# Kernel optimization log

Measured on AMD Instinct MI355X. Metric: run time of the kernel, lower is better.

The kernel has to match this reference:

```python
import jax, jax.numpy as jnp
import numpy as np
import math

IN_SRC, IN_DST, OUT, H = 64, 64, 128, 8
DK = OUT // H


def setup_inputs() -> dict:
    key = jax.random.key(0)
    ks = jax.random.split(key, 24)
    f = lambda k, shp, s=0.05: (jax.random.normal(k, shp, dtype=jnp.float32) * s)
    B, n, m = 16, 256, 128
    inp = {
        'h_dst': jax.random.normal(ks[0], (B, n, IN_DST), dtype=jnp.float32),
        'h_src': jax.random.normal(ks[1], (B, m, IN_SRC), dtype=jnp.float32),
        'h_edge': jax.random.normal(ks[2], (B, n, m), dtype=jnp.float32),
        'ope_ma_adj': jax.random.randint(ks[3], (B, n, m), 0, 2, dtype=jnp.int32),
        'ope_oo_adj': jax.random.randint(ks[4], (B, n, n), 0, 2, dtype=jnp.int32),
        'batch_idxes': jnp.arange(B, dtype=jnp.int64),
        'Wq': f(ks[5], (OUT, IN_DST)), 'bq': f(ks[6], (OUT,)),
        'Wk': f(ks[7], (OUT, IN_SRC)), 'bk': f(ks[8], (OUT,)),
        'Wkd': f(ks[9], (OUT, IN_DST)), 'bkd': f(ks[10], (OUT,)),
        'Wke': f(ks[11], (OUT, 1)), 'bke': f(ks[12], (OUT,)),
        'Wv': f(ks[13], (OUT, IN_SRC)), 'bv': f(ks[14], (OUT,)),
        'Wvd': f(ks[15], (OUT, IN_DST)), 'bvd': f(ks[16], (OUT,)),
        'Wa': f(ks[17], (OUT, OUT)), 'ba': f(ks[18], (OUT,)),
        'rel_pri': jnp.ones((2, H), dtype=jnp.float32),
        'rel_att': f(ks[19], (2, H, DK, DK), 0.2),
        'rel_msg': f(ks[20], (2, H, DK, DK), 0.2),
        'skip': jnp.ones((1,), dtype=jnp.float32),
    }
    return inp


def reference(h_dst, h_src, h_edge, ope_ma_adj, ope_oo_adj, batch_idxes,
              Wq, bq, Wk, bk, Wkd, bkd, Wke, bke, Wv, bv, Wvd, bvd, Wa, ba,
              rel_pri, rel_att, rel_msg, skip):
    B = batch_idxes.shape[0]
    n, m = h_dst.shape[1], h_src.shape[1]
    adj_ma = ope_ma_adj[batch_idxes].astype(jnp.float32)  # [B,n,m]
    adj_oo = ope_oo_adj[batch_idxes].astype(jnp.float32)  # [B,n,n]
    inv_sqrt_dk = 1.0 / math.sqrt(DK)
    # torch einsum 'abcd,abdd->abcd' multiplies by the diagonal of the relation matrix
    dA0 = jnp.diagonal(rel_att[0], axis1=-2, axis2=-1)  # [H,DK]
    dA1 = jnp.diagonal(rel_att[1], axis1=-2, axis2=-1)
    dM0 = jnp.diagonal(rel_msg[0], axis1=-2, axis2=-1)
    dM1 = jnp.diagonal(rel_msg[1], axis1=-2, axis2=-1)

    q = (h_dst @ Wq.T + bq).reshape(B, n, H, DK)           # [B,n,H,DK]
    k = ((h_src @ Wk.T + bk).reshape(B, m, H, DK)) * dA0   # [B,m,H,DK]
    scale0 = rel_pri[0] * inv_sqrt_dk                      # [H]
    m_o_att = jnp.einsum('bnhd,bmhd->bnmh', q, k) * scale0

    # edge projection: Linear(1->OUT) on h_edge[...,None]
    edge = (h_edge[..., None] * Wke[:, 0] + bke).reshape(B, n, m, H, DK) * dA0
    ee = jnp.einsum('bnhd,bnmhd->bnmh', q, edge) * scale0
    m_att = jax.nn.leaky_relu(adj_ma[..., None] * m_o_att + ee, 0.1)

    kd = ((h_dst @ Wkd.T + bkd).reshape(B, n, H, DK)) * dA1
    scale1 = rel_pri[1] * inv_sqrt_dk
    o_att = jax.nn.leaky_relu(adj_oo[..., None] * jnp.einsum('bnhd,bmhd->bnmh', q, kd) * scale1, 0.1)

    att = jnp.concatenate([m_att, o_att], axis=2)          # [B,n,m+n,H]
    mask = jnp.concatenate([adj_ma, adj_oo], axis=2)[..., None] == 1
    att = jax.nn.softmax(jnp.where(mask, att, -1e9), axis=2)
    att_m, att_o = att[:, :, :m], att[:, :, m:]

    v = ((h_src @ Wv.T + bv).reshape(B, m, H, DK)) * dM0   # [B,m,H,DK]
    # m_res_msg = edge + v[:,None]; weighted sum over m (no [B,n,m,H,DK] extra alloc)
    a_m = (jnp.einsum('bnmh,bnmhd->bnhd', att_m, edge)
           + jnp.einsum('bnmh,bmhd->bnhd', att_m, v))
    c = ((h_dst @ Wvd.T + bvd).reshape(B, n, H, DK)) * dM1
    # o_res_msg[b,i,j] = c[b,i] + c[b,j]; weighted sum over j
    a_o = (jnp.einsum('bnjh,bjhd->bnhd', att_o, c)
           + att_o.sum(axis=2)[..., None] * c)

    res = (a_m + a_o).reshape(B, n, OUT)
    trans = jax.nn.gelu(res, approximate=False) @ Wa.T + ba
    alpha = jax.nn.sigmoid(skip[0])
    out = trans * alpha + q.reshape(B, n, OUT) * (1.0 - alpha)
    return out
```

## Files before the change

### kernel.cpp

```cpp
#include <hip/hip_runtime.h>
#include <math.h>

#define H 8
#define DK 16
#define OUTC 128
#define INC 64
#define NB 16
#define NN 256
#define NM 128

typedef float f32x4 __attribute__((ext_vector_type(4)));
typedef short s16x4 __attribute__((ext_vector_type(4)));
typedef short s16x8 __attribute__((ext_vector_type(8)));

#if __has_builtin(__builtin_amdgcn_mfma_f32_16x16x16bf16_1k)
__device__ __forceinline__ f32x4 MFMA16(s16x4 a, s16x4 b, f32x4 c) {
    return __builtin_amdgcn_mfma_f32_16x16x16bf16_1k(a, b, c, 0, 0, 0);
}
#else
__device__ __forceinline__ f32x4 MFMA16(s16x4 a, s16x4 b, f32x4 c) {
    s16x8 a8 = {a[0], a[1], a[2], a[3], 0, 0, 0, 0};
    s16x8 b8 = {b[0], b[1], b[2], b[3], 0, 0, 0, 0};
    return __builtin_amdgcn_mfma_f32_16x16x32_bf16(a8, b8, c, 0, 0, 0);
}
#endif

__device__ __forceinline__ unsigned short f2bf(float x) {
    unsigned int u = __float_as_uint(x);
    return (unsigned short)((u + 0x7fffu + ((u >> 16) & 1u)) >> 16);
}
__device__ __forceinline__ float bf2f(unsigned short s) {
    return __uint_as_float(((unsigned int)s) << 16);
}

struct KArgs {
    const float* h_dst; const float* h_src; const float* h_edge;
    const int* adj_ma; const int* adj_oo;
    const float* Wq; const float* bq; const float* Wk; const float* bk;
    const float* Wkd; const float* bkd; const float* Wke; const float* bke;
    const float* Wv; const float* bv; const float* Wvd; const float* bvd;
    const float* Wa; const float* ba;
    const float* rel_pri; const float* rel_att; const float* rel_msg;
    const float* skip;
    float* qbuf; unsigned short* qpk; unsigned short* kpk; unsigned short* vpk;
    unsigned long long* mk; float* outp;
};

__global__ __launch_bounds__(256) void proj_pack_k(KArgs A)
{
    __shared__ float X_s[64 * 68];
    __shared__ float WT_s[64 * 128];

    int t = threadIdx.x;
    int unit = blockIdx.x;

    if (unit >= 256) {
        int w = ((unit - 256) << 2) + (t >> 6);
        int l = t & 63;
        #pragma unroll
        for (int i = 0; i < 16; ++i) {
            int flat = w * 16 + i;
            int row = flat / 6, g = flat - row * 6;
            int a = (g < 2) ? A.adj_ma[(long)row * NM + (g << 6) + l]
                            : A.adj_oo[(long)row * NN + ((g - 2) << 6) + l];
            unsigned long long m = __ballot(a != 0);
            if (l == 0) A.mk[flat] = m;
        }
        return;
    }

    int type, grow0;
    const float *X, *W, *bias;
    if (unit < 64)        { type = 0; grow0 = unit * 64;        X = A.h_dst; W = A.Wq;  bias = A.bq;  }
    else if (unit < 128)  { type = 2; grow0 = (unit-64) * 64;   X = A.h_dst; W = A.Wkd; bias = A.bkd; }
    else if (unit < 192)  { type = 4; grow0 = (unit-128) * 64;  X = A.h_dst; W = A.Wvd; bias = A.bvd; }
    else if (unit < 224)  { type = 1; grow0 = (unit-192) * 64;  X = A.h_src; W = A.Wk;  bias = A.bk;  }
    else                  { type = 3; grow0 = (unit-224) * 64;  X = A.h_src; W = A.Wv;  bias = A.bv;  }

    #pragma unroll
    for (int p = 0; p < 4; ++p) {
        int idx = t + 256 * p;
        int row = idx >> 4, part = idx & 15;
        float4 v = *(const float4*)(X + (long)(grow0 + row) * INC + part * 4);
        *(float4*)(X_s + row * 68 + part * 4) = v;
    }
    #pragma unroll
    for (int p = 0; p < 8; ++p) {
        int idx = t + 256 * p;
        int o = idx >> 4, part = idx & 15;
        float4 v = *(const float4*)(W + (long)o * INC + part * 4);
        int q0 = o >> 2, ob = o & 3;
        WT_s[(part*4+0)*128 + (((q0 ^ ((part*4+0)&31))<<2) + ob)] = v.x;
        WT_s[(part*4+1)*128 + (((q0 ^ ((part*4+1)&31))<<2) + ob)] = v.y;
        WT_s[(part*4+2)*128 + (((q0 ^ ((part*4+2)&31))<<2) + ob)] = v.z;
        WT_s[(part*4+3)*128 + (((q0 ^ ((part*4+3)&31))<<2) + ob)] = v.w;
    }
    __syncthreads();

    int o4 = t & 31;
    int rq = t >> 5;
    float4 acc[8];
    #pragma unroll
    for (int rr = 0; rr < 8; ++rr) acc[rr] = make_float4(0.f, 0.f, 0.f, 0.f);

    #pragma unroll 4
    for (int i4 = 0; i4 < 16; ++i4) {
        float4 w0 = *(const float4*)(WT_s + (i4*4+0)*128 + ((o4 ^ ((i4*4+0)&31))<<2));
        float4 w1 = *(const float4*)(WT_s + (i4*4+1)*128 + ((o4 ^ ((i4*4+1)&31))<<2));
        float4 w2 = *(const float4*)(WT_s + (i4*4+2)*128 + ((o4 ^ ((i4*4+2)&31))<<2));
        float4 w3 = *(const float4*)(WT_s + (i4*4+3)*128 + ((o4 ^ ((i4*4+3)&31))<<2));
        #pragma unroll
        for (int rr = 0; rr < 8; ++rr) {
            float4 x = *(const float4*)(X_s + (rq + 8*rr) * 68 + i4*4);
            acc[rr].x += x.x*w0.x + x.y*w1.x + x.z*w2.x + x.w*w3.x;
            acc[rr].y += x.x*w0.y + x.y*w1.y + x.z*w2.y + x.w*w3.y;
            acc[rr].z += x.x*w0.z + x.y*w1.z + x.z*w2.z + x.w*w3.z;
            acc[rr].w += x.x*w0.w + x.y*w1.w + x.z*w2.w + x.w*w3.w;
        }
    }

    int obase = o4 * 4;
    int head = o4 >> 2;
    float4 bs = *(const float4*)(bias + obase);
    float scl[4];
    #pragma unroll
    for (int c = 0; c < 4; ++c) {
        int o = obase + c;
        int hh = o >> 4, d = o & 15;
        float v = 1.f;
        if (type == 1)      v = A.rel_pri[hh]     * 0.25f * A.rel_att[(hh*DK + d)*DK + d];
        else if (type == 2) v = A.rel_pri[H + hh] * 0.25f * A.rel_att[((H + hh)*DK + d)*DK + d];
        else if (type == 3) v = A.rel_msg[(hh*DK + d)*DK + d];
        else if (type == 4) v = A.rel_msg[((H + hh)*DK + d)*DK + d];
        scl[c] = v;
    }
    #pragma unroll
    for (int rr = 0; rr < 8; ++rr) {
        int grow = grow0 + rq + 8*rr;
        float4 r4;
        r4.x = (acc[rr].x + bs.x) * scl[0];
        r4.y = (acc[rr].y + bs.y) * scl[1];
        r4.z = (acc[rr].z + bs.z) * scl[2];
        r4.w = (acc[rr].w + bs.w) * scl[3];
        if (type == 0) {
            *(float4*)(A.qbuf + (long)grow * OUTC + obase) = r4;
            unsigned int lo = (unsigned int)f2bf(r4.x) | ((unsigned int)f2bf(r4.y) << 16);
            unsigned int hi = (unsigned int)f2bf(r4.z) | ((unsigned int)f2bf(r4.w) << 16);
            int b = grow >> 8, row = grow & 255;
            int lane = ((o4 & 3) << 4) + (row & 15);
            ((uint2*)A.qpk)[(long)((b*H + head)*16 + (row >> 4)) * 64 + lane] = make_uint2(lo, hi);
        } else if (type == 1 || type == 2) {
            unsigned int lo = (unsigned int)f2bf(r4.x) | ((unsigned int)f2bf(r4.y) << 16);
            unsigned int hi = (unsigned int)f2bf(r4.z) | ((unsigned int)f2bf(r4.w) << 16);
            int b, key;
            if (type == 1) { b = grow >> 7; key = grow & 127; }
            else           { b = grow >> 8; key = 128 + (grow & 255); }
            int lane = (key & 15) + ((o4 & 3) << 4);
            ((uint2*)A.kpk)[(long)((b*H + head)*24 + (key >> 4)) * 64 + lane] = make_uint2(lo, hi);
        } else {
            int b, key;
            if (type == 3) { b = grow >> 7; key = grow & 127; }
            else           { b = grow >> 8; key = 128 + (grow & 255); }
            int tt = key >> 4, lg = (key >> 2) & 3, slot = key & 3;
            int dbase = (o4 & 3) * 4;
            unsigned short* vp = A.vpk + ((long)((b*H + head)*24 + tt) * 64) * 4;
            vp[(lg*16 + dbase+0)*4 + slot] = f2bf(r4.x);
            vp[(lg*16 + dbase+1)*4 + slot] = f2bf(r4.y);
            vp[(lg*16 + dbase+2)*4 + slot] = f2bf(r4.z);
            vp[(lg*16 + dbase+3)*4 + slot] = f2bf(r4.w);
        }
    }
}

__global__ __launch_bounds__(512) void attn_out_k(KArgs A)
{
    __shared__ __align__(16) unsigned char smem[73984];
    float* gel_s = (float*)smem;
    float* WaT   = (float*)(smem + 8448);
    float* he_s  = (float*)(smem + 8448);
    unsigned long long* mk_s = (unsigned long long*)(smem + 17152);
    float* s1s2_s = (float*)(smem + 17920);
    float* stats_s = (float*)(smem + 18944);

    int t = threadIdx.x;
    int bid = blockIdx.x;
    int b = bid >> 4;
    int chunk = bid & 15;
    int row0 = b * NN + chunk * 16;

    {
        int q = t >> 5, jc = (t & 31) << 2;
        float4 v = *(const float4*)(A.h_edge + (long)(row0 + q) * NM + jc);
        he_s[(jc+0)*17 + q] = v.x;
        he_s[(jc+1)*17 + q] = v.y;
        he_s[(jc+2)*17 + q] = v.z;
        he_s[(jc+3)*17 + q] = v.w;
    }
    if (t < 96) mk_s[t] = A.mk[(long)row0 * 6 + t];
    if (t < 128) {
        int row = t & 15, hh = t >> 4;
        const float* qr = A.qbuf + (long)(row0 + row) * OUTC + hh * DK;
        float s1 = 0.f, s2 = 0.f;
        #pragma unroll
        for (int d = 0; d < DK; ++d) {
            int o = hh * DK + d;
            float qq = qr[d] * A.rel_att[o * DK + d];
            s1 += qq * A.Wke[o];
            s2 += qq * A.bke[o];
        }
        float sc = A.rel_pri[hh] * 0.25f;
        s1s2_s[(hh*16 + row)*2]     = s1 * sc;
        s1s2_s[(hh*16 + row)*2 + 1] = s2 * sc;
    }
    __syncthreads();

    int w = t >> 6, l = t & 63;
    int qi = l & 15;
    int grpb = (l >> 4) << 2;
    int bh = b * H + w;

    union { uint2 u; s16x4 s; } qf;
    qf.u = ((const uint2*)A.qpk)[(long)(bh * 16 + chunk) * 64 + l];

    float S1q = s1s2_s[(w*16 + qi)*2], S2q = s1s2_s[(w*16 + qi)*2 + 1];
    unsigned int mdw[12];
    #pragma unroll
    for (int i = 0; i < 12; ++i) mdw[i] = ((const unsigned int*)(mk_s + qi * 6))[i];

    const uint2* kbase = (const uint2*)A.kpk + (long)(bh * 24) * 64;
    const uint2* vbase = (const uint2*)A.vpk + (long)(bh * 24) * 64;

    float sum = 0.f, t0 = 0.f, t1 = 0.f, so = 0.f;
    f32x4 O0 = {0.f, 0.f, 0.f, 0.f};
    f32x4 O1 = {0.f, 0.f, 0.f, 0.f};
    const f32x4 zero = {0.f, 0.f, 0.f, 0.f};

    #pragma unroll
    for (int tt = 0; tt < 24; ++tt) {
        union { uint2 u; s16x4 s; } kf, vf;
        kf.u = kbase[tt * 64 + l];
        vf.u = vbase[tt * 64 + l];
        f32x4 s4 = MFMA16(kf.s, qf.s, zero);

        unsigned int dw = mdw[tt >> 1];
        int sb = ((tt & 1) << 4) + grpb;
        float ev[4], hev[4];
        #pragma unroll
        for (int r = 0; r < 4; ++r) {
            float x = s4[r];
            if (tt < 8) {
                hev[r] = he_s[(tt * 16 + grpb + r) * 17 + qi];
                x += hev[r] * S1q + S2q;
            }
            float lk = fmaxf(x, 0.1f * x);
            float ex = __expf(lk);
            ev[r] = ((dw >> (sb + r)) & 1u) ? ex : 0.f;
        }
        float es = (ev[0] + ev[1]) + (ev[2] + ev[3]);
        sum += es;
        if (tt < 8) {
            t0 += es;
            t1 += (ev[0]*hev[0] + ev[1]*hev[1]) + (ev[2]*hev[2] + ev[3]*hev[3]);
        } else {
            so += es;
        }
        s16x4 p;
        p[0] = (short)f2bf(ev[0]); p[1] = (short)f2bf(ev[1]);
        p[2] = (short)f2bf(ev[2]); p[3] = (short)f2bf(ev[3]);
        if (tt & 1) O1 = MFMA16(p, vf.s, O1);
        else        O0 = MFMA16(p, vf.s, O0);
    }
    f32x4 O = O0 + O1;

    sum += __shfl_xor(sum, 16); sum += __shfl_xor(sum, 32);
    t0  += __shfl_xor(t0, 16);  t0  += __shfl_xor(t0, 32);
    t1  += __shfl_xor(t1, 16);  t1  += __shfl_xor(t1, 32);
    so  += __shfl_xor(so, 16);  so  += __shfl_xor(so, 32);
    if (l < 16) {
        float4 st = make_float4(1.f / sum, t0, t1, so);
        *(float4*)(stats_s + (w * 16 + l) * 4) = st;
    }

    {
        int d = qi;
        int o = w * DK + d;
        float a0 = A.rel_att[o * DK + d];
        float wk = A.Wke[o], bk = A.bke[o];
        #pragma unroll
        for (int r = 0; r < 4; ++r) {
            int ql = grpb + r;
            float4 st = *(const float4*)(stats_s + (w * 16 + ql) * 4);
            int key = 128 + chunk * 16 + ql;
            int tt = key >> 4, lg = (key >> 2) & 3, slot = key & 3;
            float cs = bf2f(A.vpk[(((long)(bh * 24) + tt) * 64 + lg*16 + d) * 4 + slot]);
            float res = st.x * (O[r] + a0 * (wk * st.z + bk * st.y) + st.w * cs);
            gel_s[ql * 132 + o] = 0.5f * res * (1.f + erff(res * 0.70710678118654752f));
        }
    }
    __syncthreads();

    #pragma unroll
    for (int p = 0; p < 8; ++p) {
        int idx = t + 512 * p;
        int o = idx >> 5, part = idx & 31;
        float4 v = *(const float4*)(A.Wa + (long)o * OUTC + part * 4);
        int q0 = o >> 2, ob = o & 3;
        WaT[(part*4+0)*128 + (((q0 ^ ((part*4+0)&31))<<2) + ob)] = v.x;
        WaT[(part*4+1)*128 + (((q0 ^ ((part*4+1)&31))<<2) + ob)] = v.y;
        WaT[(part*4+2)*128 + (((q0 ^ ((part*4+2)&31))<<2) + ob)] = v.z;
        WaT[(part*4+3)*128 + (((q0 ^ ((part*4+3)&31))<<2) + ob)] = v.w;
    }
    __syncthreads();

    {
        int o4 = t & 31, rp = t >> 5;
        float4 acc = make_float4(0.f,0.f,0.f,0.f);
        #pragma unroll 4
        for (int i4 = 0; i4 < 32; ++i4) {
            float4 w0 = *(const float4*)(WaT + (i4*4+0)*128 + ((o4 ^ ((i4*4+0)&31))<<2));
            float4 w1 = *(const float4*)(WaT + (i4*4+1)*128 + ((o4 ^ ((i4*4+1)&31))<<2));
            float4 w2 = *(const float4*)(WaT + (i4*4+2)*128 + ((o4 ^ ((i4*4+2)&31))<<2));
            float4 w3 = *(const float4*)(WaT + (i4*4+3)*128 + ((o4 ^ ((i4*4+3)&31))<<2));
            float4 x0 = *(const float4*)(gel_s + rp * 132 + i4*4);
            acc.x += x0.x*w0.x + x0.y*w1.x + x0.z*w2.x + x0.w*w3.x;
            acc.y += x0.x*w0.y + x0.y*w1.y + x0.z*w2.y + x0.w*w3.y;
            acc.z += x0.x*w0.z + x0.y*w1.z + x0.z*w2.z + x0.w*w3.z;
            acc.w += x0.x*w0.w + x0.y*w1.w + x0.z*w2.w + x0.w*w3.w;
        }

        float alpha = 1.f / (1.f + __expf(-A.skip[0]));
        float beta = 1.f - alpha;
        int obase = o4 * 4;
        float4 bs = *(const float4*)(A.ba + obase);
        float4 q0 = *(const float4*)(A.qbuf + (long)(row0 + rp) * OUTC + obase);
        float4 r0;
        r0.x = alpha*(acc.x + bs.x) + beta*q0.x;
        r0.y = alpha*(acc.y + bs.y) + beta*q0.y;
        r0.z = alpha*(acc.z + bs.z) + beta*q0.z;
        r0.w = alpha*(acc.w + bs.w) + beta*q0.w;
        *(float4*)(A.outp + (long)(row0 + rp) * OUTC + obase) = r0;
    }
}

extern "C" void kernel_launch(void* const* d_in, const int* in_sizes, int n_in,
                              void* d_out, int out_size, void* d_ws, size_t ws_size,
                              hipStream_t stream) {
    char* ws = (char*)d_ws;
    KArgs A;
    A.h_dst  = (const float*)d_in[0];
    A.h_src  = (const float*)d_in[1];
    A.h_edge = (const float*)d_in[2];
    A.adj_ma = (const int*)d_in[3];
    A.adj_oo = (const int*)d_in[4];
    A.Wq  = (const float*)d_in[6];
    A.bq  = (const float*)d_in[7];
    A.Wk  = (const float*)d_in[8];
    A.bk  = (const float*)d_in[9];
    A.Wkd = (const float*)d_in[10];
    A.bkd = (const float*)d_in[11];
    A.Wke = (const float*)d_in[12];
    A.bke = (const float*)d_in[13];
    A.Wv  = (const float*)d_in[14];
    A.bv  = (const float*)d_in[15];
    A.Wvd = (const float*)d_in[16];
    A.bvd = (const float*)d_in[17];
    A.Wa  = (const float*)d_in[18];
    A.ba  = (const float*)d_in[19];
    A.rel_pri = (const float*)d_in[20];
    A.rel_att = (const float*)d_in[21];
    A.rel_msg = (const float*)d_in[22];
    A.skip    = (const float*)d_in[23];

    A.qbuf = (float*)ws;
    A.qpk  = (unsigned short*)(ws + 2097152);
    A.kpk  = (unsigned short*)(ws + 3145728);
    A.vpk  = (unsigned short*)(ws + 4718592);
    A.mk   = (unsigned long long*)(ws + 6291456);
    A.outp = (float*)d_out;

    proj_pack_k<<<640, 256, 0, stream>>>(A);
    attn_out_k<<<NB * 16, 512, 0, stream>>>(A);
}
```

Before: 38.32 us.

## Split attention key tiles across two waves per head and use MFMA for output projection

The attention kernel now launches 1024 threads so each head gets two waves, each covering half of the key tiles, with partial outputs and softmax stats combined through shared memory. Adjacency-mask packing moves from the projection kernel into the attention kernel. The projection kernel uses 32-row tiles to double its block count. The final Wa projection switches from an fp32 LDS-transposed loop to bf16 MFMA with a split-K reduction, which drops the Wa staging but adds bf16 rounding and extra barriers.

Result: faster. 33.83 us (-11.7%).

```diff
diff --git a/kernel.cpp b/kernel.cpp
--- a/kernel.cpp
+++ b/kernel.cpp
@@ -43,42 +43,27 @@
     const float* rel_pri; const float* rel_att; const float* rel_msg;
     const float* skip;
     float* qbuf; unsigned short* qpk; unsigned short* kpk; unsigned short* vpk;
-    unsigned long long* mk; float* outp;
+    float* outp;
 };
 
-__global__ __launch_bounds__(256) void proj_pack_k(KArgs A)
+__global__ __launch_bounds__(256) void proj_k(KArgs A)
 {
-    __shared__ float X_s[64 * 68];
+    __shared__ float X_s[32 * 68];
     __shared__ float WT_s[64 * 128];
 
     int t = threadIdx.x;
     int unit = blockIdx.x;
 
-    if (unit >= 256) {
-        int w = ((unit - 256) << 2) + (t >> 6);
-        int l = t & 63;
-        #pragma unroll
-        for (int i = 0; i < 16; ++i) {
-            int flat = w * 16 + i;
-            int row = flat / 6, g = flat - row * 6;
-            int a = (g < 2) ? A.adj_ma[(long)row * NM + (g << 6) + l]
-                            : A.adj_oo[(long)row * NN + ((g - 2) << 6) + l];
-            unsigned long long m = __ballot(a != 0);
-            if (l == 0) A.mk[flat] = m;
-        }
-        return;
-    }
-
     int type, grow0;
     const float *X, *W, *bias;
-    if (unit < 64)        { type = 0; grow0 = unit * 64;        X = A.h_dst; W = A.Wq;  bias = A.bq;  }
-    else if (unit < 128)  { type = 2; grow0 = (unit-64) * 64;   X = A.h_dst; W = A.Wkd; bias = A.bkd; }
-    else if (unit < 192)  { type = 4; grow0 = (unit-128) * 64;  X = A.h_dst; W = A.Wvd; bias = A.bvd; }
-    else if (unit < 224)  { type = 1; grow0 = (unit-192) * 64;  X = A.h_src; W = A.Wk;  bias = A.bk;  }
-    else                  { type = 3; grow0 = (unit-224) * 64;  X = A.h_src; W = A.Wv;  bias = A.bv;  }
-
-    #pragma unroll
-    for (int p = 0; p < 4; ++p) {
+    if (unit < 128)       { type = 0; grow0 = unit * 32;        X = A.h_dst; W = A.Wq;  bias = A.bq;  }
+    else if (unit < 256)  { type = 2; grow0 = (unit-128) * 32;  X = A.h_dst; W = A.Wkd; bias = A.bkd; }
+    else if (unit < 384)  { type = 4; grow0 = (unit-256) * 32;  X = A.h_dst; W = A.Wvd; bias = A.bvd; }
+    else if (unit < 448)  { type = 1; grow0 = (unit-384) * 32;  X = A.h_src; W = A.Wk;  bias = A.bk;  }
+    else                  { type = 3; grow0 = (unit-448) * 32;  X = A.h_src; W = A.Wv;  bias = A.bv;  }
+
+    #pragma unroll
+    for (int p = 0; p < 2; ++p) {
         int idx = t + 256 * p;
         int row = idx >> 4, part = idx & 15;
         float4 v = *(const float4*)(X + (long)(grow0 + row) * INC + part * 4);
@@ -99,9 +84,9 @@
 
     int o4 = t & 31;
     int rq = t >> 5;
-    float4 acc[8];
-    #pragma unroll
-    for (int rr = 0; rr < 8; ++rr) acc[rr] = make_float4(0.f, 0.f, 0.f, 0.f);
+    float4 acc[4];
+    #pragma unroll
+    for (int rr = 0; rr < 4; ++rr) acc[rr] = make_float4(0.f, 0.f, 0.f, 0.f);
 
     #pragma unroll 4
     for (int i4 = 0; i4 < 16; ++i4) {
@@ -110,7 +95,7 @@
         float4 w2 = *(const float4*)(WT_s + (i4*4+2)*128 + ((o4 ^ ((i4*4+2)&31))<<2));
         float4 w3 = *(const float4*)(WT_s + (i4*4+3)*128 + ((o4 ^ ((i4*4+3)&31))<<2));
         #pragma unroll
-        for (int rr = 0; rr < 8; ++rr) {
+        for (int rr = 0; rr < 4; ++rr) {
             float4 x = *(const float4*)(X_s + (rq + 8*rr) * 68 + i4*4);
             acc[rr].x += x.x*w0.x + x.y*w1.x + x.z*w2.x + x.w*w3.x;
             acc[rr].y += x.x*w0.y + x.y*w1.y + x.z*w2.y + x.w*w3.y;
@@ -135,7 +120,7 @@
         scl[c] = v;
     }
     #pragma unroll
-    for (int rr = 0; rr < 8; ++rr) {
+    for (int rr = 0; rr < 4; ++rr) {
         int grow = grow0 + rq + 8*rr;
         float4 r4;
         r4.x = (acc[rr].x + bs.x) * scl[0];
@@ -172,15 +157,16 @@
     }
 }
 
-__global__ __launch_bounds__(512) void attn_out_k(KArgs A)
+__global__ __launch_bounds__(1024) void attn_out_k(KArgs A)
 {
-    __shared__ __align__(16) unsigned char smem[73984];
-    float* gel_s = (float*)smem;
-    float* WaT   = (float*)(smem + 8448);
-    float* he_s  = (float*)(smem + 8448);
+    __shared__ __align__(16) unsigned char smem[37376];
+    float* gel_s  = (float*)smem;
+    float* he_s   = (float*)(smem + 8448);
     unsigned long long* mk_s = (unsigned long long*)(smem + 17152);
     float* s1s2_s = (float*)(smem + 17920);
-    float* stats_s = (float*)(smem + 18944);
+    float* stats_s= (float*)(smem + 18944);
+    float* ocomb  = (float*)(smem + 20992);
+    float* scomb  = (float*)(smem + 29184);
 
     int t = threadIdx.x;
     int bid = blockIdx.x;
@@ -188,7 +174,9 @@
     int chunk = bid & 15;
     int row0 = b * NN + chunk * 16;
 
-    {
+    int w = t >> 6, l = t & 63;
+
+    if (t < 512) {
         int q = t >> 5, jc = (t & 31) << 2;
         float4 v = *(const float4*)(A.h_edge + (long)(row0 + q) * NM + jc);
         he_s[(jc+0)*17 + q] = v.x;
@@ -196,7 +184,15 @@
         he_s[(jc+2)*17 + q] = v.z;
         he_s[(jc+3)*17 + q] = v.w;
     }
-    if (t < 96) mk_s[t] = A.mk[(long)row0 * 6 + t];
+    {
+        #pragma unroll
+        for (int g = 0; g < 6; ++g) {
+            int a = (g < 2) ? A.adj_ma[(long)(row0 + w) * NM + (g << 6) + l]
+                            : A.adj_oo[(long)(row0 + w) * NN + ((g - 2) << 6) + l];
+            unsigned long long m = __ballot(a != 0);
+            if (l == 0) mk_s[w * 6 + g] = m;
+        }
+    }
     if (t < 128) {
         int row = t & 15, hh = t >> 4;
         const float* qr = A.qbuf + (long)(row0 + row) * OUTC + hh * DK;
@@ -214,15 +210,15 @@
     }
     __syncthreads();
 
-    int w = t >> 6, l = t & 63;
+    int head = w & 7, half = w >> 3;
     int qi = l & 15;
     int grpb = (l >> 4) << 2;
-    int bh = b * H + w;
+    int bh = b * H + head;
 
     union { uint2 u; s16x4 s; } qf;
     qf.u = ((const uint2*)A.qpk)[(long)(bh * 16 + chunk) * 64 + l];
 
-    float S1q = s1s2_s[(w*16 + qi)*2], S2q = s1s2_s[(w*16 + qi)*2 + 1];
+    float S1q = s1s2_s[(head*16 + qi)*2], S2q = s1s2_s[(head*16 + qi)*2 + 1];
     unsigned int mdw[12];
     #pragma unroll
     for (int i = 0; i < 12; ++i) mdw[i] = ((const unsigned int*)(mk_s + qi * 6))[i];
@@ -234,21 +230,22 @@
     f32x4 O0 = {0.f, 0.f, 0.f, 0.f};
     f32x4 O1 = {0.f, 0.f, 0.f, 0.f};
     const f32x4 zero = {0.f, 0.f, 0.f, 0.f};
-
-    #pragma unroll
-    for (int tt = 0; tt < 24; ++tt) {
+    int sb = (half << 4) + grpb;
+
+    #pragma unroll
+    for (int i = 0; i < 12; ++i) {
+        int tt = 2 * i + half;
         union { uint2 u; s16x4 s; } kf, vf;
         kf.u = kbase[tt * 64 + l];
         vf.u = vbase[tt * 64 + l];
         f32x4 s4 = MFMA16(kf.s, qf.s, zero);
 
-        unsigned int dw = mdw[tt >> 1];
-        int sb = ((tt & 1) << 4) + grpb;
+        unsigned int dw = mdw[i];
         float ev[4], hev[4];
         #pragma unroll
         for (int r = 0; r < 4; ++r) {
             float x = s4[r];
-            if (tt < 8) {
+            if (i < 4) {
                 hev[r] = he_s[(tt * 16 + grpb + r) * 17 + qi];
                 x += hev[r] * S1q + S2q;
             }
@@ -258,7 +255,7 @@
         }
         float es = (ev[0] + ev[1]) + (ev[2] + ev[3]);
         sum += es;
-        if (tt < 8) {
+        if (i < 4) {
             t0 += es;
             t1 += (ev[0]*hev[0] + ev[1]*hev[1]) + (ev[2]*hev[2] + ev[3]*hev[3]);
         } else {
@@ -267,78 +264,81 @@
         s16x4 p;
         p[0] = (short)f2bf(ev[0]); p[1] = (short)f2bf(ev[1]);
         p[2] = (short)f2bf(ev[2]); p[3] = (short)f2bf(ev[3]);
-        if (tt & 1) O1 = MFMA16(p, vf.s, O1);
-        else        O0 = MFMA16(p, vf.s, O0);
-    }
-    f32x4 O = O0 + O1;
-
-    sum += __shfl_xor(sum, 16); sum += __shfl_xor(sum, 32);
-    t0  += __shfl_xor(t0, 16);  t0  += __shfl_xor(t0, 32);
-    t1  += __shfl_xor(t1, 16);  t1  += __shfl_xor(t1, 32);
-    so  += __shfl_xor(so, 16);  so  += __shfl_xor(so, 32);
-    if (l < 16) {
-        float4 st = make_float4(1.f / sum, t0, t1, so);
-        *(float4*)(stats_s + (w * 16 + l) * 4) = st;
-    }
-
-    {
+        if (i & 1) O1 = MFMA16(p, vf.s, O1);
+        else       O0 = MFMA16(p, vf.s, O0);
+    }
+    f32x4 Op = O0 + O1;
+
+    if (half) {
+        *(f32x4*)(ocomb + (head*64 + l)*4) = Op;
+        float4 sc4 = make_float4(sum, t0, t1, so);
+        *(float4*)(scomb + (head*64 + l)*4) = sc4;
+    }
+    __syncthreads();
+
+    if (!half) {
+        f32x4 Oo = *(const f32x4*)(ocomb + (head*64 + l)*4);
+        float4 sc4 = *(const float4*)(scomb + (head*64 + l)*4);
+        f32x4 O = Op + Oo;
+        sum += sc4.x; t0 += sc4.y; t1 += sc4.z; so += sc4.w;
+
+        sum += __shfl_xor(sum, 16); sum += __shfl_xor(sum, 32);
+        t0  += __shfl_xor(t0, 16);  t0  += __shfl_xor(t0, 32);
+        t1  += __shfl_xor(t1, 16);  t1  += __shfl_xor(t1, 32);
+        so  += __shfl_xor(so, 16);  so  += __shfl_xor(so, 32);
+        if (l < 16) {
+            float4 st = make_float4(1.f / sum, t0, t1, so);
+            *(float4*)(stats_s + (head * 16 + l) * 4) = st;
+        }
+
         int d = qi;
-        int o = w * DK + d;
+        int o = head * DK + d;
         float a0 = A.rel_att[o * DK + d];
         float wk = A.Wke[o], bk = A.bke[o];
         #pragma unroll
         for (int r = 0; r < 4; ++r) {
             int ql = grpb + r;
-            float4 st = *(const float4*)(stats_s + (w * 16 + ql) * 4);
+            float4 st = *(const float4*)(stats_s + (head * 16 + ql) * 4);
             int key = 128 + chunk * 16 + ql;
-            int tt = key >> 4, lg = (key >> 2) & 3, slot = key & 3;
-            float cs = bf2f(A.vpk[(((long)(bh * 24) + tt) * 64 + lg*16 + d) * 4 + slot]);
+            int tk = key >> 4, lg = (key >> 2) & 3, slot = key & 3;
+            float cs = bf2f(A.vpk[(((long)(bh * 24) + tk) * 64 + lg*16 + d) * 4 + slot]);
             float res = st.x * (O[r] + a0 * (wk * st.z + bk * st.y) + st.w * cs);
             gel_s[ql * 132 + o] = 0.5f * res * (1.f + erff(res * 0.70710678118654752f));
         }
     }
     __syncthreads();
 
-    #pragma unroll
-    for (int p = 0; p < 8; ++p) {
-        int idx = t + 512 * p;
-        int o = idx >> 5, part = idx & 31;
-        float4 v = *(const float4*)(A.Wa + (long)o * OUTC + part * 4);
-        int q0 = o >> 2, ob = o & 3;
-        WaT[(part*4+0)*128 + (((q0 ^ ((part*4+0)&31))<<2) + ob)] = v.x;
-        WaT[(part*4+1)*128 + (((q0 ^ ((part*4+1)&31))<<2) + ob)] = v.y;
-        WaT[(part*4+2)*128 + (((q0 ^ ((part*4+2)&31))<<2) + ob)] = v.z;
-        WaT[(part*4+3)*128 + (((q0 ^ ((part*4+3)&31))<<2) + ob)] = v.w;
-    }
-    __syncthreads();
-
     {
-        int o4 = t & 31, rp = t >> 5;
-        float4 acc = make_float4(0.f,0.f,0.f,0.f);
-        #pragma unroll 4
-        for (int i4 = 0; i4 < 32; ++i4) {
-            float4 w0 = *(const float4*)(WaT + (i4*4+0)*128 + ((o4 ^ ((i4*4+0)&31))<<2));
-            float4 w1 = *(const float4*)(WaT + (i4*4+1)*128 + ((o4 ^ ((i4*4+1)&31))<<2));
-            float4 w2 = *(const float4*)(WaT + (i4*4+2)*128 + ((o4 ^ ((i4*4+2)&31))<<2));
-            float4 w3 = *(const float4*)(WaT + (i4*4+3)*128 + ((o4 ^ ((i4*4+3)&31))<<2));
-            float4 x0 = *(const float4*)(gel_s + rp * 132 + i4*4);
-            acc.x += x0.x*w0.x + x0.y*w1.x + x0.z*w2.x + x0.w*w3.x;
-            acc.y += x0.x*w0.y + x0.y*w1.y + x0.z*w2.y + x0.w*w3.y;
-            acc.z += x0.x*w0.z + x0.y*w1.z + x0.z*w2.z + x0.w*w3.z;
-            acc.w += x0.x*w0.w + x0.y*w1.w + x0.z*w2.w + x0.w*w3.w;
-        }
-
-        float alpha = 1.f / (1.f + __expf(-A.skip[0]));
-        float beta = 1.f - alpha;
-        int obase = o4 * 4;
-        float4 bs = *(const float4*)(A.ba + obase);
-        float4 q0 = *(const float4*)(A.qbuf + (long)(row0 + rp) * OUTC + obase);
-        float4 r0;
-        r0.x = alpha*(acc.x + bs.x) + beta*q0.x;
-        r0.y = alpha*(acc.y + bs.y) + beta*q0.y;
-        r0.z = alpha*(acc.z + bs.z) + beta*q0.z;
-        r0.w = alpha*(acc.w + bs.w) + beta*q0.w;
-        *(float4*)(A.outp + (long)(row0 + rp) * OUTC + obase) = r0;
+        int ct = head, kh = half;
+        f32x4 Cp = {0.f, 0.f, 0.f, 0.f};
+        #pragma unroll
+        for (int kk = 0; kk < 4; ++kk) {
+            int kt = kh * 4 + kk;
+            float4 ga = *(const float4*)(gel_s + (l & 15) * 132 + kt * 16 + grpb);
+            float4 wb = *(const float4*)(A.Wa + (long)(ct * 16 + (l & 15)) * OUTC + kt * 16 + grpb);
+            s16x4 af, bf;
+            af[0] = (short)f2bf(ga.x); af[1] = (short)f2bf(ga.y);
+            af[2] = (short)f2bf(ga.z); af[3] = (short)f2bf(ga.w);
+            bf[0] = (short)f2bf(wb.x); bf[1] = (short)f2bf(wb.y);
+            bf[2] = (short)f2bf(wb.z); bf[3] = (short)f2bf(wb.w);
+            Cp = MFMA16(af, bf, Cp);
+        }
+        if (kh) *(f32x4*)(ocomb + (ct*64 + l)*4) = Cp;
+        __syncthreads();
+        if (!kh) {
+            f32x4 Co = *(const f32x4*)(ocomb + (ct*64 + l)*4);
+            Cp = Cp + Co;
+            float alpha = 1.f / (1.f + __expf(-A.skip[0]));
+            float beta = 1.f - alpha;
+            int co = ct * 16 + (l & 15);
+            float bias = A.ba[co];
+            #pragma unroll
+            for (int r = 0; r < 4; ++r) {
+                long grow = row0 + grpb + r;
+                float q0 = A.qbuf[grow * OUTC + co];
+                A.outp[grow * OUTC + co] = alpha * (Cp[r] + bias) + beta * q0;
+            }
+        }
     }
 }
 
@@ -375,9 +375,8 @@
     A.qpk  = (unsigned short*)(ws + 2097152);
     A.kpk  = (unsigned short*)(ws + 3145728);
     A.vpk  = (unsigned short*)(ws + 4718592);
-    A.mk   = (unsigned long long*)(ws + 6291456);
     A.outp = (float*)d_out;
 
-    proj_pack_k<<<640, 256, 0, stream>>>(A);
-    attn_out_k<<<NB * 16, 512, 0, stream>>>(A);
-}
+    proj_k<<<512, 256, 0, stream>>>(A);
+    attn_out_k<<<NB * 16, 1024, 0, stream>>>(A);
+}
```
